# Optimization experiments

Measured on AMD Instinct MI355X. Metric: run time of the kernel, lower is better.

Reference implementation:

```python
import jax, jax.numpy as jnp
import numpy as np

B, N, D, U, S = 32, 1024, 2, 64, 2


def setup_inputs() -> dict:
    key = jax.random.key(0)
    ks = jax.random.split(key, 8)
    scale = 1.0 / np.sqrt(N)  # keep diffusion outputs in a sane range
    inputs = jax.random.normal(ks[0], (B, N, D), jnp.float32)
    supports = jax.random.normal(ks[1], (B, N, N, S), jnp.float32) * scale
    h_prev = jax.random.normal(ks[2], (B, N * U), jnp.float32)
    rows = (D + U) * (S + 1)  # 198
    wscale = 1.0 / np.sqrt(rows)
    r_kernel = jax.random.normal(ks[3], (rows, U), jnp.float32) * wscale
    u_kernel = jax.random.normal(ks[4], (rows, U), jnp.float32) * wscale
    c_kernel = jax.random.normal(ks[5], (rows, U), jnp.float32) * wscale
    zeros = jnp.zeros((U,), jnp.float32)
    return {"inputs": inputs, "supports": supports, "h_prev": h_prev,
            "r_kernel": r_kernel, "r_bias": zeros,
            "u_kernel": u_kernel, "u_bias": zeros,
            "c_kernel": c_kernel, "c_bias": zeros}


def _diff_conv(x_in, supports, state, kernel, bias):
    # x_in: (B,N,D), state: (B, N*U) -> output (B, N*U)
    b, n, _ = x_in.shape
    u = kernel.shape[1]
    x0 = jnp.concatenate([x_in, state.reshape(b, n, u)], axis=-1)  # (B,N,F)
    # batched graph diffusion for all S supports at once: (B,N,N,S)x(B,N,F)->(B,N,F,S)
    xm = jnp.einsum('bijs,bjf->bifs', supports, x0)
    x = jnp.concatenate([x0[..., None], xm], axis=-1)  # (B,N,F,M) matches tf stack+transpose order
    x = x.reshape(b * n, -1) @ kernel + bias  # (B*N, U)
    return x.reshape(b, n * u)


def reference(inputs, supports, h_prev, r_kernel, r_bias, u_kernel, u_bias, c_kernel, c_bias):
    r = jax.nn.sigmoid(_diff_conv(inputs, supports, h_prev, r_kernel, r_bias))
    u = jax.nn.sigmoid(_diff_conv(inputs, supports, h_prev, u_kernel, u_bias))
    c = jnp.tanh(_diff_conv(inputs, supports, r * h_prev, c_kernel, c_bias))
    h = u * h_prev + (1.0 - u) * c
    return h
```

## Files before the change

### kernel.cpp

```cpp
#include <hip/hip_runtime.h>
#include <hip/hip_bf16.h>

namespace {

constexpr int kN  = 1024;
constexpr int kU  = 64;
constexpr int kFP = 80;

typedef __attribute__((ext_vector_type(4))) float f32x4;
typedef __attribute__((ext_vector_type(8))) short sv8;
typedef unsigned int u32;
typedef unsigned short u16;

__device__ __forceinline__ u32 pack_bf2(float a, float b) {
  __hip_bfloat16 ha = __float2bfloat16(a);
  __hip_bfloat16 hb = __float2bfloat16(b);
  u16 ua = *reinterpret_cast<u16*>(&ha);
  u16 ub = *reinterpret_cast<u16*>(&hb);
  return (u32)ua | ((u32)ub << 16);
}

__device__ __forceinline__ u16 bf16bits(float a) {
  __hip_bfloat16 h = __float2bfloat16(a);
  return *reinterpret_cast<u16*>(&h);
}

__device__ __forceinline__ float bflo(u32 v) {
  u32 x = v << 16;
  return *reinterpret_cast<float*>(&x);
}
__device__ __forceinline__ float bfhi(u32 v) {
  u32 x = v & 0xffff0000u;
  return *reinterpret_cast<float*>(&x);
}

__device__ __forceinline__ void gl16(const void* g, void* l) {
  __builtin_amdgcn_global_load_lds(
      (const __attribute__((address_space(1))) u32*)g,
      (__attribute__((address_space(3))) u32*)l, 16, 0, 0);
}

__global__ __launch_bounds__(256) void convert_sup(
    const f32x4* __restrict__ sup4, u16* __restrict__ supb) {
  const int bx = blockIdx.x;
  const int b  = bx >> 6;
  const int rg = bx & 63;
  const int tile = rg >> 2, w = rg & 3;
  const int t  = threadIdx.x;
  const int l64 = t & 63, tg = t >> 6;
  const int T2 = l64 >> 5, ks = (l64 >> 4) & 1, q = (l64 >> 2) & 3;
  const int e  = (l64 & 3) * 2;

  __shared__ u16 CL[4096];

  const size_t rowbase = (size_t)(b * 1024 + rg * 16) * 512;
  u16* const outbase =
      supb + ((size_t)((b * 16 + tile) * 2)) * 65536 + w * 512;

#pragma unroll 1
  for (int jc = 0; jc < 8; ++jc) {
    f32x4 v0 = __builtin_nontemporal_load(sup4 + rowbase + (size_t)(tg) * 512 + jc * 64 + l64);
    f32x4 v1 = __builtin_nontemporal_load(sup4 + rowbase + (size_t)(tg + 4) * 512 + jc * 64 + l64);
    f32x4 v2 = __builtin_nontemporal_load(sup4 + rowbase + (size_t)(tg + 8) * 512 + jc * 64 + l64);
    f32x4 v3 = __builtin_nontemporal_load(sup4 + rowbase + (size_t)(tg + 12) * 512 + jc * 64 + l64);
    const int ob = T2 * 1024 + ks * 512 + q * 8 + e;
    *reinterpret_cast<u32*>(&CL[ob + (tg) * 32])           = pack_bf2(v0[0], v0[2]);
    *reinterpret_cast<u32*>(&CL[2048 + ob + (tg) * 32])    = pack_bf2(v0[1], v0[3]);
    *reinterpret_cast<u32*>(&CL[ob + (tg + 4) * 32])       = pack_bf2(v1[0], v1[2]);
    *reinterpret_cast<u32*>(&CL[2048 + ob + (tg + 4) * 32])= pack_bf2(v1[1], v1[3]);
    *reinterpret_cast<u32*>(&CL[ob + (tg + 8) * 32])       = pack_bf2(v2[0], v2[2]);
    *reinterpret_cast<u32*>(&CL[2048 + ob + (tg + 8) * 32])= pack_bf2(v2[1], v2[3]);
    *reinterpret_cast<u32*>(&CL[ob + (tg + 12) * 32])      = pack_bf2(v3[0], v3[2]);
    *reinterpret_cast<u32*>(&CL[2048 + ob + (tg + 12) * 32])= pack_bf2(v3[1], v3[3]);
    __syncthreads();
#pragma unroll
    for (int pi2 = 0; pi2 < 2; ++pi2) {
      int pi = tg + pi2 * 4;
      int so = pi >> 2, T2o = (pi >> 1) & 1, kso = pi & 1;
      uint4 d = *reinterpret_cast<const uint4*>(
          &CL[so * 2048 + T2o * 1024 + kso * 512 + (l64 & 15) * 32 + (l64 >> 4) * 8]);
      u16* dst = outbase + (size_t)so * 65536 + (jc * 2 + T2o) * 4096 +
                 kso * 2048 + (size_t)l64 * 8;
      *reinterpret_cast<uint4*>(dst) = d;
    }
    __syncthreads();
  }
}

__global__ __launch_bounds__(256) void build_x0t(
    const float* __restrict__ inputs, const float* __restrict__ h_prev,
    __hip_bfloat16* __restrict__ x0t, __hip_bfloat16* __restrict__ x0tc) {
  const int bx = blockIdx.x;
  const int b  = bx >> 4;
  const int n0 = (bx & 15) * 64;
  const int t  = threadIdx.x;

  __shared__ float hp[64][65];

  const float* hpg = h_prev + (size_t)b * kN * kU + (size_t)n0 * kU;
#pragma unroll
  for (int r = 0; r < 16; ++r) {
    int idx = t + (r << 8);
    hp[idx >> 6][idx & 63] = hpg[idx];
  }
  __syncthreads();

  {
    int u = t >> 2, g = t & 3;
    __hip_bfloat16* dst = x0t + ((size_t)b * kFP + 2 + u) * kN + n0 + g * 16;
#pragma unroll
    for (int k = 0; k < 16; ++k) dst[k] = __float2bfloat16(hp[g * 16 + k][u]);
  }

  if (t < 128) {
    int d = t & 1, nn = t >> 1;
    float v = inputs[((size_t)b * kN + n0 + nn) * 2 + d];
    __hip_bfloat16 bv = __float2bfloat16(v);
    x0t [((size_t)b * kFP + d) * kN + n0 + nn] = bv;
    x0tc[((size_t)b * kFP + d) * kN + n0 + nn] = bv;
  } else {
    int i2 = t - 128;
    __hip_bfloat16 z = __float2bfloat16(0.0f);
#pragma unroll
    for (int r = 0; r < 7; ++r) {
      int idx = i2 + r * 128;
      int row = 66 + (idx >> 6), nn = idx & 63;
      x0t [((size_t)b * kFP + row) * kN + n0 + nn] = z;
      x0tc[((size_t)b * kFP + row) * kN + n0 + nn] = z;
    }
  }
}

__global__ __launch_bounds__(512) void einsum_diff(
    const u16* __restrict__ supb, const __hip_bfloat16* __restrict__ x0t,
    u16* __restrict__ xfeat) {
  const int bx = blockIdx.x;
  const int wk = (bx & 7) * 64 + (bx >> 3);
  const int b    = wk >> 4;
  const int tile = wk & 15;
  const int i0   = tile * 64;
  const int t    = threadIdx.x;
  const int lane = t & 63;
  const int ww   = t >> 6;
  const int q    = lane >> 4;
  const int lm   = lane & 15;
  const int s    = ww & 1;
  const int ih   = ww >> 1;

  __shared__ u16 Af[2][2][2][4][64][8];
  __shared__ u16 Xf[2][10][64][8];

  f32x4 acc[5];
#pragma unroll
  for (int n = 0; n < 5; ++n) acc[n] = (f32x4){0.f, 0.f, 0.f, 0.f};

  const u16* asrc = supb + ((size_t)((b * 16 + tile) * 2 + s)) * 65536 +
                    ih * 512 + (size_t)lane * 8;
  const u16* xg = reinterpret_cast<const u16*>(x0t) + (size_t)b * kFP * kN;
  const int seg1 = ww;
  const int seg2 = ww + 8;
  const u16* xs1 =
      xg + (size_t)((seg1 % 5) * 16 + lm) * kN + (seg1 / 5) * 32 + q * 8;
  const u16* xs2 = (ww < 2)
      ? xg + (size_t)((seg2 % 5) * 16 + lm) * kN + (seg2 / 5) * 32 + q * 8
      : nullptr;

  auto dma = [&](int nb, int T) {
    gl16(asrc + T * 4096,        &Af[nb][s][0][ih][0][0]);
    gl16(asrc + T * 4096 + 2048, &Af[nb][s][1][ih][0][0]);
    gl16(xs1 + T * 64, &Xf[nb][seg1][0][0]);
    if (ww < 2) gl16(xs2 + T * 64, &Xf[nb][seg2][0][0]);
  };

  auto compute = [&](int nb) {
#pragma unroll
    for (int ks = 0; ks < 2; ++ks) {
      sv8 a = *reinterpret_cast<const sv8*>(&Af[nb][s][ks][ih][lane][0]);
#pragma unroll
      for (int n = 0; n < 5; ++n) {
        sv8 xb = *reinterpret_cast<const sv8*>(&Xf[nb][ks * 5 + n][lane][0]);
        acc[n] = __builtin_amdgcn_mfma_f32_16x16x32_bf16(a, xb, acc[n], 0, 0, 0);
      }
    }
  };

  dma(0, 0);
  asm volatile("s_waitcnt vmcnt(0)" ::: "memory");
  __builtin_amdgcn_s_barrier();
  __builtin_amdgcn_sched_barrier(0);

#pragma unroll 1
  for (int T = 0; T < 16; ++T) {
    if (T + 1 <= 15) {
      dma((T + 1) & 1, T + 1);
      if (ww < 2) { asm volatile("s_waitcnt vmcnt(4)" ::: "memory"); }
      else        { asm volatile("s_waitcnt vmcnt(3)" ::: "memory"); }
    } else {
      asm volatile("s_waitcnt vmcnt(0)" ::: "memory");
    }
    __builtin_amdgcn_s_barrier();
    __builtin_amdgcn_sched_barrier(0);
    compute(T & 1);
    __builtin_amdgcn_s_barrier();
    __builtin_amdgcn_sched_barrier(0);
  }

  u16* ep = &Af[0][0][0][0][0][0];
#pragma unroll
  for (int n = 0; n < 5; ++n) {
    int f = n * 16 + lm;
    if (f < 66) {
#pragma unroll
      for (int r = 0; r < 4; ++r) {
        int row = ih * 16 + q * 4 + r;
        ep[row * 136 + s * 66 + f] = bf16bits(acc[n][r]);
      }
    }
  }
  __syncthreads();
  const u32* ep32 = reinterpret_cast<const u32*>(ep);
  u32* og = reinterpret_cast<u32*>(xfeat) + ((size_t)b * kN + i0) * 66;
#pragma unroll 1
  for (int g = t; g < 4224; g += 512) {
    int row = g / 66, c = g - row * 66;
    og[g] = ep32[row * 68 + c];
  }
}

__global__ __launch_bounds__(256) void gates_ru(
    const u16* __restrict__ xfeat, const float* __restrict__ rk,
    const float* __restrict__ rbias, const float* __restrict__ uk,
    const float* __restrict__ ubias, const float* __restrict__ inputs,
    const float* __restrict__ h_prev, float* __restrict__ u_buf,
    __hip_bfloat16* __restrict__ x0tc) {
  const int row0 = blockIdx.x * 32;
  const int b = row0 >> 10, n0 = row0 & 1023;
  const int t = threadIdx.x;
  __shared__ float xm[32][134];
  __shared__ float x0s[32][66];

  {
    const u32* xsrc = reinterpret_cast<const u32*>(xfeat) + (size_t)row0 * 66;
#pragma unroll 1
    for (int g = t; g < 2112; g += 256) {
      int row = g / 66, c = g - row * 66;
      u32 v = xsrc[g];
      xm[row][c * 2]     = bflo(v);
      xm[row][c * 2 + 1] = bfhi(v);
    }
  }
#pragma unroll
  for (int r2 = 0; r2 < 8; ++r2) {
    int idx = t + (r2 << 8);
    int rw = idx >> 6, u = idx & 63;
    x0s[rw][2 + u] = h_prev[(size_t)(row0 + rw) * kU + u];
  }
  if (t < 64) x0s[t >> 1][t & 1] = inputs[(size_t)row0 * 2 + t];
  __syncthreads();

  const int cu = t & 15;
  const int rw = (t >> 4) * 2;
  float ar[2][4] = {{0.f,0.f,0.f,0.f},{0.f,0.f,0.f,0.f}};
  float au[2][4] = {{0.f,0.f,0.f,0.f},{0.f,0.f,0.f,0.f}};

#pragma unroll 4
  for (int f = 0; f < 66; ++f) {
    float4 vr = *reinterpret_cast<const float4*>(rk + (size_t)(f * 3) * kU + cu * 4);
    float4 vu = *reinterpret_cast<const float4*>(uk + (size_t)(f * 3) * kU + cu * 4);
    float a0 = x0s[rw][f], a1 = x0s[rw + 1][f];
    ar[0][0] += a0 * vr.x; ar[0][1] += a0 * vr.y; ar[0][2] += a0 * vr.z; ar[0][3] += a0 * vr.w;
    ar[1][0] += a1 * vr.x; ar[1][1] += a1 * vr.y; ar[1][2] += a1 * vr.z; ar[1][3] += a1 * vr.w;
    au[0][0] += a0 * vu.x; au[0][1] += a0 * vu.y; au[0][2] += a0 * vu.z; au[0][3] += a0 * vu.w;
    au[1][0] += a1 * vu.x; au[1][1] += a1 * vu.y; au[1][2] += a1 * vu.z; au[1][3] += a1 * vu.w;
  }
#pragma unroll
  for (int m = 1; m <= 2; ++m) {
#pragma unroll 4
    for (int f = 0; f < 66; ++f) {
      float4 vr = *reinterpret_cast<const float4*>(rk + (size_t)(f * 3 + m) * kU + cu * 4);
      float4 vu = *reinterpret_cast<const float4*>(uk + (size_t)(f * 3 + m) * kU + cu * 4);
      float a0 = xm[rw][(m - 1) * 66 + f], a1 = xm[rw + 1][(m - 1) * 66 + f];
      ar[0][0] += a0 * vr.x; ar[0][1] += a0 * vr.y; ar[0][2] += a0 * vr.z; ar[0][3] += a0 * vr.w;
      ar[1][0] += a1 * vr.x; ar[1][1] += a1 * vr.y; ar[1][2] += a1 * vr.z; ar[1][3] += a1 * vr.w;
      au[0][0] += a0 * vu.x; au[0][1] += a0 * vu.y; au[0][2] += a0 * vu.z; au[0][3] += a0 * vu.w;
      au[1][0] += a1 * vu.x; au[1][1] += a1 * vu.y; au[1][2] += a1 * vu.z; au[1][3] += a1 * vu.w;
    }
  }

#pragma unroll
  for (int rr = 0; rr < 2; ++rr) {
    int grow = row0 + rw + rr;
    int n = n0 + rw + rr;
#pragma unroll
    for (int j = 0; j < 4; ++j) {
      int u = cu * 4 + j;
      float rv = 1.f / (1.f + __expf(-(ar[rr][j] + rbias[u])));
      float uv = 1.f / (1.f + __expf(-(au[rr][j] + ubias[u])));
      u_buf[(size_t)grow * kU + u] = uv;
      float rh = rv * h_prev[(size_t)grow * kU + u];
      x0tc[((size_t)b * kFP + 2 + u) * kN + n] = __float2bfloat16(rh);
    }
  }
}

__global__ __launch_bounds__(256) void gate_c_final(
    const u16* __restrict__ xfeat, const float* __restrict__ ck,
    const float* __restrict__ cbias, const float* __restrict__ inputs,
    const __hip_bfloat16* __restrict__ x0tc, const float* __restrict__ h_prev,
    const float* __restrict__ u_buf, float* __restrict__ out) {
  const int row0 = blockIdx.x * 32;
  const int b = row0 >> 10, n0 = row0 & 1023;
  const int t = threadIdx.x;
  __shared__ float xm[32][134];
  __shared__ float x0c[32][66];

  {
    const u32* xsrc = reinterpret_cast<const u32*>(xfeat) + (size_t)row0 * 66;
#pragma unroll 1
    for (int g = t; g < 2112; g += 256) {
      int row = g / 66, c = g - row * 66;
      u32 v = xsrc[g];
      xm[row][c * 2]     = bflo(v);
      xm[row][c * 2 + 1] = bfhi(v);
    }
  }
#pragma unroll
  for (int r2 = 0; r2 < 8; ++r2) {
    int idx = t + (r2 << 8);
    int u = idx >> 5, nn = idx & 31;
    x0c[nn][2 + u] =
        __bfloat162float(x0tc[((size_t)b * kFP + 2 + u) * kN + n0 + nn]);
  }
  if (t < 64) x0c[t >> 1][t & 1] = inputs[(size_t)row0 * 2 + t];
  __syncthreads();

  const int cu = t & 15;
  const int rw = (t >> 4) * 2;
  float ac[2][4] = {{0.f,0.f,0.f,0.f},{0.f,0.f,0.f,0.f}};

#pragma unroll 4
  for (int f = 0; f < 66; ++f) {
    float4 vc = *reinterpret_cast<const float4*>(ck + (size_t)(f * 3) * kU + cu * 4);
    float a0 = x0c[rw][f], a1 = x0c[rw + 1][f];
    ac[0][0] += a0 * vc.x; ac[0][1] += a0 * vc.y; ac[0][2] += a0 * vc.z; ac[0][3] += a0 * vc.w;
    ac[1][0] += a1 * vc.x; ac[1][1] += a1 * vc.y; ac[1][2] += a1 * vc.z; ac[1][3] += a1 * vc.w;
  }
#pragma unroll
  for (int m = 1; m <= 2; ++m) {
#pragma unroll 4
    for (int f = 0; f < 66; ++f) {
      float4 vc = *reinterpret_cast<const float4*>(ck + (size_t)(f * 3 + m) * kU + cu * 4);
      float a0 = xm[rw][(m - 1) * 66 + f], a1 = xm[rw + 1][(m - 1) * 66 + f];
      ac[0][0] += a0 * vc.x; ac[0][1] += a0 * vc.y; ac[0][2] += a0 * vc.z; ac[0][3] += a0 * vc.w;
      ac[1][0] += a1 * vc.x; ac[1][1] += a1 * vc.y; ac[1][2] += a1 * vc.z; ac[1][3] += a1 * vc.w;
    }
  }

#pragma unroll
  for (int rr = 0; rr < 2; ++rr) {
    int grow = row0 + rw + rr;
#pragma unroll
    for (int j = 0; j < 4; ++j) {
      int u = cu * 4 + j;
      float cv = tanhf(ac[rr][j] + cbias[u]);
      float uv = u_buf[(size_t)grow * kU + u];
      float hp = h_prev[(size_t)grow * kU + u];
      out[(size_t)grow * kU + u] = uv * hp + (1.f - uv) * cv;
    }
  }
}

}

extern "C" void kernel_launch(void* const* d_in, const int* in_sizes, int n_in,
                              void* d_out, int out_size, void* d_ws, size_t ws_size,
                              hipStream_t stream) {
  const float* inputs = (const float*)d_in[0];
  const float* sup    = (const float*)d_in[1];
  const float* h_prev = (const float*)d_in[2];
  const float* rk     = (const float*)d_in[3];
  const float* rbias  = (const float*)d_in[4];
  const float* uk     = (const float*)d_in[5];
  const float* ubias  = (const float*)d_in[6];
  const float* ck     = (const float*)d_in[7];
  const float* cbias  = (const float*)d_in[8];
  float* out = (float*)d_out;

  char* ws = (char*)d_ws;
  __hip_bfloat16* x0t   = (__hip_bfloat16*)(ws);
  __hip_bfloat16* x0tc  = (__hip_bfloat16*)(ws + 5242880);
  u16*            xfeat = (u16*)(ws + 10485760);
  float*          u_buf = (float*)(ws + 19136512);
  u16*            supb  = (u16*)(ws + 27525120);

  hipLaunchKernelGGL(convert_sup, dim3(2048), dim3(256), 0, stream,
                     (const f32x4*)sup, supb);
  hipLaunchKernelGGL(build_x0t, dim3(512), dim3(256), 0, stream,
                     inputs, h_prev, x0t, x0tc);
  hipLaunchKernelGGL(einsum_diff, dim3(512), dim3(512), 0, stream,
                     supb, x0t, xfeat);
  hipLaunchKernelGGL(gates_ru, dim3(1024), dim3(256), 0, stream,
                     xfeat, rk, rbias, uk, ubias, inputs, h_prev, u_buf, x0tc);
  hipLaunchKernelGGL(einsum_diff, dim3(512), dim3(512), 0, stream,
                     supb, x0tc, xfeat);
  hipLaunchKernelGGL(gate_c_final, dim3(1024), dim3(256), 0, stream,
                     xfeat, ck, cbias, inputs, x0tc, h_prev, u_buf, out);
}
```

Before: 215.0 us.

## Pre-swizzle diffusion state into MFMA fragment layout and load operands directly to registers

The transposed state buffer is now written in the exact MFMA B-fragment order, so einsum_diff can read A and X operands straight from global memory into registers. This replaces the LDS double-buffered global_load_lds pipeline and its barriers. Each block now handles one support instead of two, using 256 threads and twice as many blocks. The gate kernel also writes a row-major bf16 r*h buffer that the final kernel reads contiguously, replacing strided transposed reads. The trade is losing explicit prefetch overlap and LDS sharing of X across waves, so X fragments are read redundantly from global/L2 memory.

```diff
diff --git a/kernel.cpp b/kernel.cpp
--- a/kernel.cpp
+++ b/kernel.cpp
@@ -5,7 +5,6 @@
 
 constexpr int kN  = 1024;
 constexpr int kU  = 64;
-constexpr int kFP = 80;
 
 typedef __attribute__((ext_vector_type(4))) float f32x4;
 typedef __attribute__((ext_vector_type(8))) short sv8;
@@ -25,6 +24,11 @@
   return *reinterpret_cast<u16*>(&h);
 }
 
+__device__ __forceinline__ float bfu(u16 v) {
+  u32 x = (u32)v << 16;
+  return *reinterpret_cast<float*>(&x);
+}
+
 __device__ __forceinline__ float bflo(u32 v) {
   u32 x = v << 16;
   return *reinterpret_cast<float*>(&x);
@@ -32,12 +36,6 @@
 __device__ __forceinline__ float bfhi(u32 v) {
   u32 x = v & 0xffff0000u;
   return *reinterpret_cast<float*>(&x);
-}
-
-__device__ __forceinline__ void gl16(const void* g, void* l) {
-  __builtin_amdgcn_global_load_lds(
-      (const __attribute__((address_space(1))) u32*)g,
-      (__attribute__((address_space(3))) u32*)l, 16, 0, 0);
 }
 
 __global__ __launch_bounds__(256) void convert_sup(
@@ -64,13 +62,13 @@
     f32x4 v2 = __builtin_nontemporal_load(sup4 + rowbase + (size_t)(tg + 8) * 512 + jc * 64 + l64);
     f32x4 v3 = __builtin_nontemporal_load(sup4 + rowbase + (size_t)(tg + 12) * 512 + jc * 64 + l64);
     const int ob = T2 * 1024 + ks * 512 + q * 8 + e;
-    *reinterpret_cast<u32*>(&CL[ob + (tg) * 32])           = pack_bf2(v0[0], v0[2]);
-    *reinterpret_cast<u32*>(&CL[2048 + ob + (tg) * 32])    = pack_bf2(v0[1], v0[3]);
-    *reinterpret_cast<u32*>(&CL[ob + (tg + 4) * 32])       = pack_bf2(v1[0], v1[2]);
-    *reinterpret_cast<u32*>(&CL[2048 + ob + (tg + 4) * 32])= pack_bf2(v1[1], v1[3]);
-    *reinterpret_cast<u32*>(&CL[ob + (tg + 8) * 32])       = pack_bf2(v2[0], v2[2]);
-    *reinterpret_cast<u32*>(&CL[2048 + ob + (tg + 8) * 32])= pack_bf2(v2[1], v2[3]);
-    *reinterpret_cast<u32*>(&CL[ob + (tg + 12) * 32])      = pack_bf2(v3[0], v3[2]);
+    *reinterpret_cast<u32*>(&CL[ob + (tg) * 32])            = pack_bf2(v0[0], v0[2]);
+    *reinterpret_cast<u32*>(&CL[2048 + ob + (tg) * 32])     = pack_bf2(v0[1], v0[3]);
+    *reinterpret_cast<u32*>(&CL[ob + (tg + 4) * 32])        = pack_bf2(v1[0], v1[2]);
+    *reinterpret_cast<u32*>(&CL[2048 + ob + (tg + 4) * 32]) = pack_bf2(v1[1], v1[3]);
+    *reinterpret_cast<u32*>(&CL[ob + (tg + 8) * 32])        = pack_bf2(v2[0], v2[2]);
+    *reinterpret_cast<u32*>(&CL[2048 + ob + (tg + 8) * 32]) = pack_bf2(v2[1], v2[3]);
+    *reinterpret_cast<u32*>(&CL[ob + (tg + 12) * 32])       = pack_bf2(v3[0], v3[2]);
     *reinterpret_cast<u32*>(&CL[2048 + ob + (tg + 12) * 32])= pack_bf2(v3[1], v3[3]);
     __syncthreads();
 #pragma unroll
@@ -89,10 +87,11 @@
 
 __global__ __launch_bounds__(256) void build_x0t(
     const float* __restrict__ inputs, const float* __restrict__ h_prev,
-    __hip_bfloat16* __restrict__ x0t, __hip_bfloat16* __restrict__ x0tc) {
+    u16* __restrict__ xt, u16* __restrict__ xtc) {
   const int bx = blockIdx.x;
   const int b  = bx >> 4;
-  const int n0 = (bx & 15) * 64;
+  const int T  = bx & 15;
+  const int n0 = T * 64;
   const int t  = threadIdx.x;
 
   __shared__ float hp[64][65];
@@ -105,125 +104,82 @@
   }
   __syncthreads();
 
-  {
-    int u = t >> 2, g = t & 3;
-    __hip_bfloat16* dst = x0t + ((size_t)b * kFP + 2 + u) * kN + n0 + g * 16;
-#pragma unroll
-    for (int k = 0; k < 16; ++k) dst[k] = __float2bfloat16(hp[g * 16 + k][u]);
-  }
-
-  if (t < 128) {
-    int d = t & 1, nn = t >> 1;
-    float v = inputs[((size_t)b * kN + n0 + nn) * 2 + d];
-    __hip_bfloat16 bv = __float2bfloat16(v);
-    x0t [((size_t)b * kFP + d) * kN + n0 + nn] = bv;
-    x0tc[((size_t)b * kFP + d) * kN + n0 + nn] = bv;
-  } else {
-    int i2 = t - 128;
-    __hip_bfloat16 z = __float2bfloat16(0.0f);
-#pragma unroll
-    for (int r = 0; r < 7; ++r) {
-      int idx = i2 + r * 128;
-      int row = 66 + (idx >> 6), nn = idx & 63;
-      x0t [((size_t)b * kFP + row) * kN + n0 + nn] = z;
-      x0tc[((size_t)b * kFP + row) * kN + n0 + nn] = z;
-    }
-  }
-}
-
-__global__ __launch_bounds__(512) void einsum_diff(
-    const u16* __restrict__ supb, const __hip_bfloat16* __restrict__ x0t,
+  u16* xtb  = xt  + ((size_t)(b * 16 + T) * 10) * 512;
+  u16* xtcb = xtc + ((size_t)(b * 16 + T) * 10) * 512;
+
+#pragma unroll 1
+  for (int idx = t; idx < 5120; idx += 256) {
+    int f = idx >> 6, j = idx & 63;
+    int ks = j >> 5, qq = (j >> 3) & 3, e = j & 7;
+    int off = (ks * 5 + (f >> 4)) * 512 + (qq * 16 + (f & 15)) * 8 + e;
+    u16 v;
+    if (f < 2)       v = bf16bits(inputs[((size_t)(b << 10) + n0 + j) * 2 + f]);
+    else if (f < 66) v = bf16bits(hp[j][f - 2]);
+    else             v = 0;
+    xtb[off] = v;
+    if (f < 2)        xtcb[off] = v;
+    else if (f >= 66) xtcb[off] = 0;
+  }
+}
+
+__global__ __launch_bounds__(256, 4) void einsum_diff(
+    const u16* __restrict__ supb, const u16* __restrict__ xt,
     u16* __restrict__ xfeat) {
   const int bx = blockIdx.x;
-  const int wk = (bx & 7) * 64 + (bx >> 3);
-  const int b    = wk >> 4;
-  const int tile = wk & 15;
+  const int wk = (bx & 7) * 128 + (bx >> 3);
+  const int b    = wk >> 5;
+  const int rem  = wk & 31;
+  const int tile = rem >> 1;
+  const int s    = rem & 1;
   const int i0   = tile * 64;
   const int t    = threadIdx.x;
   const int lane = t & 63;
-  const int ww   = t >> 6;
+  const int w    = t >> 6;
   const int q    = lane >> 4;
   const int lm   = lane & 15;
-  const int s    = ww & 1;
-  const int ih   = ww >> 1;
-
-  __shared__ u16 Af[2][2][2][4][64][8];
-  __shared__ u16 Xf[2][10][64][8];
+
+  __shared__ u16 ep[64][68];
 
   f32x4 acc[5];
 #pragma unroll
   for (int n = 0; n < 5; ++n) acc[n] = (f32x4){0.f, 0.f, 0.f, 0.f};
 
   const u16* asrc = supb + ((size_t)((b * 16 + tile) * 2 + s)) * 65536 +
-                    ih * 512 + (size_t)lane * 8;
-  const u16* xg = reinterpret_cast<const u16*>(x0t) + (size_t)b * kFP * kN;
-  const int seg1 = ww;
-  const int seg2 = ww + 8;
-  const u16* xs1 =
-      xg + (size_t)((seg1 % 5) * 16 + lm) * kN + (seg1 / 5) * 32 + q * 8;
-  const u16* xs2 = (ww < 2)
-      ? xg + (size_t)((seg2 % 5) * 16 + lm) * kN + (seg2 / 5) * 32 + q * 8
-      : nullptr;
-
-  auto dma = [&](int nb, int T) {
-    gl16(asrc + T * 4096,        &Af[nb][s][0][ih][0][0]);
-    gl16(asrc + T * 4096 + 2048, &Af[nb][s][1][ih][0][0]);
-    gl16(xs1 + T * 64, &Xf[nb][seg1][0][0]);
-    if (ww < 2) gl16(xs2 + T * 64, &Xf[nb][seg2][0][0]);
-  };
-
-  auto compute = [&](int nb) {
-#pragma unroll
-    for (int ks = 0; ks < 2; ++ks) {
-      sv8 a = *reinterpret_cast<const sv8*>(&Af[nb][s][ks][ih][lane][0]);
-#pragma unroll
-      for (int n = 0; n < 5; ++n) {
-        sv8 xb = *reinterpret_cast<const sv8*>(&Xf[nb][ks * 5 + n][lane][0]);
-        acc[n] = __builtin_amdgcn_mfma_f32_16x16x32_bf16(a, xb, acc[n], 0, 0, 0);
-      }
-    }
-  };
-
-  dma(0, 0);
-  asm volatile("s_waitcnt vmcnt(0)" ::: "memory");
-  __builtin_amdgcn_s_barrier();
-  __builtin_amdgcn_sched_barrier(0);
+                    w * 512 + (size_t)lane * 8;
+  const u16* xb = xt + (size_t)(b * 16) * 5120 + (size_t)lane * 8;
 
 #pragma unroll 1
   for (int T = 0; T < 16; ++T) {
-    if (T + 1 <= 15) {
-      dma((T + 1) & 1, T + 1);
-      if (ww < 2) { asm volatile("s_waitcnt vmcnt(4)" ::: "memory"); }
-      else        { asm volatile("s_waitcnt vmcnt(3)" ::: "memory"); }
-    } else {
-      asm volatile("s_waitcnt vmcnt(0)" ::: "memory");
-    }
-    __builtin_amdgcn_s_barrier();
-    __builtin_amdgcn_sched_barrier(0);
-    compute(T & 1);
-    __builtin_amdgcn_s_barrier();
-    __builtin_amdgcn_sched_barrier(0);
-  }
-
-  u16* ep = &Af[0][0][0][0][0][0];
+    sv8 a0 = *reinterpret_cast<const sv8*>(asrc + T * 4096);
+    sv8 a1 = *reinterpret_cast<const sv8*>(asrc + T * 4096 + 2048);
+    sv8 X[10];
+#pragma unroll
+    for (int seg = 0; seg < 10; ++seg)
+      X[seg] = *reinterpret_cast<const sv8*>(xb + T * 5120 + seg * 512);
+#pragma unroll
+    for (int n = 0; n < 5; ++n)
+      acc[n] = __builtin_amdgcn_mfma_f32_16x16x32_bf16(a0, X[n], acc[n], 0, 0, 0);
+#pragma unroll
+    for (int n = 0; n < 5; ++n)
+      acc[n] = __builtin_amdgcn_mfma_f32_16x16x32_bf16(a1, X[5 + n], acc[n], 0, 0, 0);
+  }
+
 #pragma unroll
   for (int n = 0; n < 5; ++n) {
     int f = n * 16 + lm;
     if (f < 66) {
 #pragma unroll
-      for (int r = 0; r < 4; ++r) {
-        int row = ih * 16 + q * 4 + r;
-        ep[row * 136 + s * 66 + f] = bf16bits(acc[n][r]);
-      }
+      for (int r = 0; r < 4; ++r)
+        ep[w * 16 + q * 4 + r][f] = bf16bits(acc[n][r]);
     }
   }
   __syncthreads();
-  const u32* ep32 = reinterpret_cast<const u32*>(ep);
-  u32* og = reinterpret_cast<u32*>(xfeat) + ((size_t)b * kN + i0) * 66;
-#pragma unroll 1
-  for (int g = t; g < 4224; g += 512) {
-    int row = g / 66, c = g - row * 66;
-    og[g] = ep32[row * 68 + c];
+  const u32* ep32 = reinterpret_cast<const u32*>(&ep[0][0]);
+  u32* og = reinterpret_cast<u32*>(xfeat) + ((size_t)b * kN + i0) * 66 + s * 33;
+#pragma unroll 1
+  for (int g = t; g < 2112; g += 256) {
+    int row = g / 33, c = g - row * 33;
+    og[(size_t)row * 66 + c] = ep32[row * 34 + c];
   }
 }
 
@@ -232,7 +188,7 @@
     const float* __restrict__ rbias, const float* __restrict__ uk,
     const float* __restrict__ ubias, const float* __restrict__ inputs,
     const float* __restrict__ h_prev, float* __restrict__ u_buf,
-    __hip_bfloat16* __restrict__ x0tc) {
+    u16* __restrict__ xtc, u16* __restrict__ rh) {
   const int row0 = blockIdx.x * 32;
   const int b = row0 >> 10, n0 = row0 & 1023;
   const int t = threadIdx.x;
@@ -291,14 +247,21 @@
   for (int rr = 0; rr < 2; ++rr) {
     int grow = row0 + rw + rr;
     int n = n0 + rw + rr;
-#pragma unroll
-    for (int j = 0; j < 4; ++j) {
-      int u = cu * 4 + j;
-      float rv = 1.f / (1.f + __expf(-(ar[rr][j] + rbias[u])));
-      float uv = 1.f / (1.f + __expf(-(au[rr][j] + ubias[u])));
+    int T = n >> 6, j = n & 63;
+    int ks = j >> 5, qq = (j >> 3) & 3, e = j & 7;
+    size_t chunk = ((size_t)(b * 16 + T) * 10) * 512;
+#pragma unroll
+    for (int jj = 0; jj < 4; ++jj) {
+      int u = cu * 4 + jj;
+      float rv = 1.f / (1.f + __expf(-(ar[rr][jj] + rbias[u])));
+      float uv = 1.f / (1.f + __expf(-(au[rr][jj] + ubias[u])));
       u_buf[(size_t)grow * kU + u] = uv;
-      float rh = rv * h_prev[(size_t)grow * kU + u];
-      x0tc[((size_t)b * kFP + 2 + u) * kN + n] = __float2bfloat16(rh);
+      float rhv = rv * h_prev[(size_t)grow * kU + u];
+      u16 rb16 = bf16bits(rhv);
+      rh[(size_t)grow * kU + u] = rb16;
+      int f = 2 + u;
+      xtc[chunk + (size_t)((ks * 5 + (f >> 4)) * 512 +
+                           (qq * 16 + (f & 15)) * 8 + e)] = rb16;
     }
   }
 }
@@ -306,10 +269,9 @@
 __global__ __launch_bounds__(256) void gate_c_final(
     const u16* __restrict__ xfeat, const float* __restrict__ ck,
     const float* __restrict__ cbias, const float* __restrict__ inputs,
-    const __hip_bfloat16* __restrict__ x0tc, const float* __restrict__ h_prev,
+    const u16* __restrict__ rh, const float* __restrict__ h_prev,
     const float* __restrict__ u_buf, float* __restrict__ out) {
   const int row0 = blockIdx.x * 32;
-  const int b = row0 >> 10, n0 = row0 & 1023;
   const int t = threadIdx.x;
   __shared__ float xm[32][134];
   __shared__ float x0c[32][66];
@@ -327,9 +289,8 @@
 #pragma unroll
   for (int r2 = 0; r2 < 8; ++r2) {
     int idx = t + (r2 << 8);
-    int u = idx >> 5, nn = idx & 31;
-    x0c[nn][2 + u] =
-        __bfloat162float(x0tc[((size_t)b * kFP + 2 + u) * kN + n0 + nn]);
+    int rw2 = idx >> 6, u = idx & 63;
+    x0c[rw2][2 + u] = bfu(rh[(size_t)(row0 + rw2) * kU + u]);
   }
   if (t < 64) x0c[t >> 1][t & 1] = inputs[(size_t)row0 * 2 + t];
   __syncthreads();
@@ -387,22 +348,23 @@
   float* out = (float*)d_out;
 
   char* ws = (char*)d_ws;
-  __hip_bfloat16* x0t   = (__hip_bfloat16*)(ws);
-  __hip_bfloat16* x0tc  = (__hip_bfloat16*)(ws + 5242880);
-  u16*            xfeat = (u16*)(ws + 10485760);
-  float*          u_buf = (float*)(ws + 19136512);
-  u16*            supb  = (u16*)(ws + 27525120);
+  u16*   xt    = (u16*)(ws);
+  u16*   xtc   = (u16*)(ws + 5242880);
+  u16*   xfeat = (u16*)(ws + 10485760);
+  float* u_buf = (float*)(ws + 19136512);
+  u16*   rh    = (u16*)(ws + 27525120);
+  u16*   supb  = (u16*)(ws + 31719424);
 
   hipLaunchKernelGGL(convert_sup, dim3(2048), dim3(256), 0, stream,
                      (const f32x4*)sup, supb);
   hipLaunchKernelGGL(build_x0t, dim3(512), dim3(256), 0, stream,
-                     inputs, h_prev, x0t, x0tc);
-  hipLaunchKernelGGL(einsum_diff, dim3(512), dim3(512), 0, stream,
-                     supb, x0t, xfeat);
+                     inputs, h_prev, xt, xtc);
+  hipLaunchKernelGGL(einsum_diff, dim3(1024), dim3(256), 0, stream,
+                     supb, xt, xfeat);
   hipLaunchKernelGGL(gates_ru, dim3(1024), dim3(256), 0, stream,
-                     xfeat, rk, rbias, uk, ubias, inputs, h_prev, u_buf, x0tc);
-  hipLaunchKernelGGL(einsum_diff, dim3(512), dim3(512), 0, stream,
-                     supb, x0tc, xfeat);
+                     xfeat, rk, rbias, uk, ubias, inputs, h_prev, u_buf, xtc, rh);
+  hipLaunchKernelGGL(einsum_diff, dim3(1024), dim3(256), 0, stream,
+                     supb, xtc, xfeat);
   hipLaunchKernelGGL(gate_c_final, dim3(1024), dim3(256), 0, stream,
-                     xfeat, ck, cbias, inputs, x0tc, h_prev, u_buf, out);
-}
+                     xfeat, ck, cbias, inputs, rh, h_prev, u_buf, out);
+}
```

Result: slower. 232.4 us (+8.1%).
